# Kernel tuning notes

Hardware: AMD Instinct MI355X
Metric: run time of the kernel (lower is better)

Reference implementation:

```python
import jax, jax.numpy as jnp
import numpy as np

N_NODES = 100000
N_EDGES = 1600000
D_IN = 128
D_HID = 128
D_OUT = 64
N_GRAPHS = 128


def setup_inputs() -> dict:
    key = jax.random.key(0)
    ks = jax.random.split(key, 8)
    x = jax.random.normal(ks[0], (N_NODES, D_IN), dtype=jnp.float32)
    edge_index = jax.random.randint(ks[1], (2, N_EDGES), 0, N_NODES, dtype=jnp.int64)
    batch = jnp.sort(jax.random.randint(ks[2], (N_NODES,), 0, N_GRAPHS, dtype=jnp.int64))
    def glorot(k, fi, fo):
        s = jnp.sqrt(6.0 / (fi + fo)).astype(jnp.float32)
        return jax.random.uniform(k, (fi, fo), jnp.float32, -1.0, 1.0) * s
    return {
        "x": x, "edge_index": edge_index, "batch": batch,
        "W1": glorot(ks[3], D_IN, D_HID), "b1": jnp.zeros((D_HID,), jnp.float32),
        "W2": glorot(ks[4], D_HID, D_HID), "b2": jnp.zeros((D_HID,), jnp.float32),
        "W3": glorot(ks[5], D_HID, D_HID), "b3": jnp.zeros((D_HID,), jnp.float32),
        "Wfc": glorot(ks[6], D_HID, D_OUT), "bfc": jnp.zeros((D_OUT,), jnp.float32),
    }


def _gcn_graph(edge_index, n_nodes):
    # add self-loops and compute symmetric normalization (PyG gcn_norm)
    loop = jnp.arange(n_nodes, dtype=edge_index.dtype)
    src = jnp.concatenate([edge_index[0], loop])
    dst = jnp.concatenate([edge_index[1], loop])
    deg = jax.ops.segment_sum(jnp.ones_like(dst, dtype=jnp.float32), dst,
                              num_segments=n_nodes)
    dinv = jnp.where(deg > 0, jax.lax.rsqrt(deg), 0.0)
    norm = dinv[src] * dinv[dst]  # [E + N]
    return src, dst, norm


def _gcn_conv(x, src, dst, norm, W, b, n_nodes):
    h = x @ W                                    # [N, F_out]
    msg = h[src] * norm[:, None]                 # gather + scale
    agg = jax.ops.segment_sum(msg, dst, num_segments=n_nodes)  # scatter-add
    return agg + b


def reference(x, edge_index, batch, W1, b1, W2, b2, W3, b3, Wfc, bfc):
    n = x.shape[0]
    src, dst, norm = _gcn_graph(edge_index, n)
    h = jax.nn.relu(_gcn_conv(x, src, dst, norm, W1, b1, n))
    h = jax.nn.relu(_gcn_conv(h, src, dst, norm, W2, b2, n))
    h = jax.nn.relu(_gcn_conv(h, src, dst, norm, W3, b3, n))
    # global mean pool over graphs in the batch
    sums = jax.ops.segment_sum(h, batch, num_segments=N_GRAPHS)
    cnts = jax.ops.segment_sum(jnp.ones((n,), jnp.float32), batch,
                               num_segments=N_GRAPHS)
    pooled = sums / jnp.maximum(cnts, 1.0)[:, None]   # [G, D_HID]
    return pooled @ Wfc + bfc                         # [G, D_OUT]
```

## Files before the change

### kernel.cpp

```cpp
#include <hip/hip_runtime.h>

#define NN 100000
#define NE 1600000
#define DF 128
#define DOUT 64
#define NG 128
#define NB 391
#define EPB 2048
#define NBLKA ((NE + EPB - 1) / EPB)
#define NBLKX 6250
#define PCH 8
#define NAGB (NN / 16)

typedef short short8 __attribute__((ext_vector_type(8)));
typedef float floatx4 __attribute__((ext_vector_type(4)));
typedef float floatx2 __attribute__((ext_vector_type(2)));

__device__ __forceinline__ unsigned short f2bf(float f) {
    unsigned int b = __float_as_uint(f);
    unsigned int r = (b + 0x7fffu + ((b >> 16) & 1u)) >> 16;
    return (unsigned short)r;
}
__device__ __forceinline__ float bf2f_lo(unsigned int v) { return __uint_as_float(v << 16); }
__device__ __forceinline__ float bf2f_hi(unsigned int v) { return __uint_as_float(v & 0xffff0000u); }

__device__ __forceinline__ int phi(int p) {
    return (((p >> 6) << 2) + (p & 3)) * 16 + ((p >> 2) & 15);
}


__global__ __launch_bounds__(256) void k_init(int* __restrict__ bhist,
                                              const int* __restrict__ batch,
                                              int* __restrict__ gstart,
                                              const float* __restrict__ W1,
                                              const float* __restrict__ W2,
                                              const float* __restrict__ W3,
                                              unsigned short* __restrict__ O1,
                                              unsigned short* __restrict__ O2,
                                              unsigned short* __restrict__ O3) {
    int blk = blockIdx.x;
    if (blk < 2) {
        int i = blk * 256 + threadIdx.x;
        if (i < NB) bhist[i] = 0;
    } else if (blk == 2) {
        int g = threadIdx.x;
        if (g > NG) return;
        int lo = 0, hi = NN;
        while (lo < hi) {
            int mid = (lo + hi) >> 1;
            if (batch[mid] < g) lo = mid + 1; else hi = mid;
        }
        gstart[g] = lo;
    } else {
        int bb = blk - 3;
        const float* W = (bb >= 16) ? W3 : (bb >= 8) ? W2 : W1;
        unsigned short* O = (bb >= 16) ? O3 : (bb >= 8) ? O2 : O1;
        int idx = (bb & 7) * 256 + threadIdx.x;
        int l = idx & 63;
        int s = (idx >> 6) & 3;
        int tt = idx >> 8;
        int k0 = s * 32 + (l >> 4) * 8;
        int c = tt * 16 + (l & 15);
        unsigned short o[8];
#pragma unroll
        for (int j = 0; j < 8; j++) o[j] = f2bf(W[phi(k0 + j) * DF + c]);
        *(short8*)&O[idx * 8] = *(short8*)o;
    }
}


__global__ __launch_bounds__(256) void k_pre(const int* __restrict__ dst,
                                             int* __restrict__ bhist,
                                             const float* __restrict__ x,
                                             unsigned short* __restrict__ xb) {
    __shared__ int lh[NB];
    int t = threadIdx.x;
    if (blockIdx.x < NBLKA) {
        for (int i = t; i < NB; i += 256) lh[i] = 0;
        __syncthreads();
        int e0 = blockIdx.x * EPB;
        int e1 = min(e0 + EPB, NE);
        for (int e = e0 + t; e < e1; e += 256) atomicAdd(&lh[dst[e] >> 8], 1);
        __syncthreads();
        for (int i = t; i < NB; i += 256) {
            int c = lh[i];
            if (c) atomicAdd(&bhist[i], c);
        }
    } else {
        size_t i = ((size_t)(blockIdx.x - NBLKA) * 256 + t) * 8;
        size_t rb = i & ~(size_t)127;
        int p0 = (int)(i & 127);
        unsigned short o[8];
#pragma unroll
        for (int j = 0; j < 8; j++) o[j] = f2bf(x[rb + phi(p0 + j)]);
        *(short8*)&xb[i] = *(short8*)o;
    }
}

__global__ __launch_bounds__(512) void k_bscan(const int* __restrict__ bhist,
                                               int* __restrict__ bbase,
                                               int* __restrict__ bcur) {
    __shared__ int sh[512];
    int t = threadIdx.x;
    int v = (t < NB) ? bhist[t] : 0;
    sh[t] = v;
    __syncthreads();
    for (int off = 1; off < 512; off <<= 1) {
        int a = (t >= off) ? sh[t - off] : 0;
        __syncthreads();
        sh[t] += a;
        __syncthreads();
    }
    if (t < NB) {
        bbase[t] = sh[t] - v;
        bcur[t] = sh[t] - v;
    }
    if (t == NB - 1) bbase[NB] = sh[t];
}

__global__ __launch_bounds__(256) void k_pairs(const int* __restrict__ src,
                                               const int* __restrict__ dst,
                                               int* __restrict__ bcur,
                                               int2* __restrict__ ebuf) {
    __shared__ int lh[NB];
    __shared__ int lbase[NB];
    int t = threadIdx.x;
    for (int i = t; i < NB; i += 256) lh[i] = 0;
    __syncthreads();
    int e0 = blockIdx.x * EPB;
    int e1 = min(e0 + EPB, NE);
    for (int e = e0 + t; e < e1; e += 256) atomicAdd(&lh[dst[e] >> 8], 1);
    __syncthreads();
    for (int i = t; i < NB; i += 256) {
        int c = lh[i];
        lbase[i] = c ? atomicAdd(&bcur[i], c) : 0;
    }
    __syncthreads();
    for (int i = t; i < NB; i += 256) lh[i] = 0;
    __syncthreads();
    for (int e = e0 + t; e < e1; e += 256) {
        int s = src[e], d = dst[e];
        int bk = d >> 8;
        int off = atomicAdd(&lh[bk], 1);
        ebuf[lbase[bk] + off] = make_int2(s, d);
    }
}

__global__ __launch_bounds__(256) void k_build(const int2* __restrict__ ebuf,
                                               const int* __restrict__ bbase,
                                               int* __restrict__ rowptr,
                                               float* __restrict__ dinv,
                                               int* __restrict__ col) {
    __shared__ int deg[256];
    __shared__ int lst[256];
    int b = blockIdx.x, t = threadIdx.x;
    int n0 = b << 8;
    int node = n0 + t;
    deg[t] = 0;
    __syncthreads();
    int e0 = bbase[b], e1 = bbase[b + 1];
    for (int e = e0 + t; e < e1; e += 256) atomicAdd(&deg[ebuf[e].y - n0], 1);
    __syncthreads();
    int v = deg[t];
    lst[t] = v;
    __syncthreads();
    for (int off = 1; off < 256; off <<= 1) {
        int a = (t >= off) ? lst[t - off] : 0;
        __syncthreads();
        lst[t] += a;
        __syncthreads();
    }
    int mystart = e0 + lst[t] - v;
    if (node < NN) {
        rowptr[node] = mystart;
        dinv[node] = rsqrtf((float)(v + 1));
    }
    if (b == NB - 1 && t == 255) rowptr[NN] = e1;
    lst[t] = mystart;
    __syncthreads();
    for (int e = e0 + t; e < e1; e += 256) {
        int2 pr = ebuf[e];
        int p = atomicAdd(&lst[pr.y - n0], 1);
        col[p] = pr.x * DF;
    }
}


__global__ __launch_bounds__(256) void k_gemm(const unsigned short* __restrict__ X,
                                              const unsigned short* __restrict__ Wb,
                                              const float* __restrict__ dinv,
                                              unsigned char* __restrict__ fs8) {
    int t = threadIdx.x;
    int wave = t >> 6, l = t & 63;
    int r0 = blockIdx.x * 64 + wave * 16;
    int lm = l & 15, q = l >> 4;

    int arow = r0 + lm;
    if (arow >= NN) arow = NN - 1;
    const unsigned short* xrow = X + (size_t)arow * DF + q * 8;
    short8 af0 = *(const short8*)(xrow);
    short8 af1 = *(const short8*)(xrow + 32);
    short8 af2 = *(const short8*)(xrow + 64);
    short8 af3 = *(const short8*)(xrow + 96);

    int orow = r0 + q * 4;
    float dv[4];
#pragma unroll
    for (int j = 0; j < 4; j++) dv[j] = (orow + j < NN) ? dinv[orow + j] : 0.f;

    float res[4][8];
#pragma unroll
    for (int tt = 0; tt < 8; tt++) {
        floatx4 acc = {0.f, 0.f, 0.f, 0.f};
        const unsigned short* wp = Wb + ((size_t)(tt * 4) * 64 + l) * 8;
        acc = __builtin_amdgcn_mfma_f32_16x16x32_bf16(af0, *(const short8*)(wp), acc, 0, 0, 0);
        acc = __builtin_amdgcn_mfma_f32_16x16x32_bf16(af1, *(const short8*)(wp + 512), acc, 0, 0, 0);
        acc = __builtin_amdgcn_mfma_f32_16x16x32_bf16(af2, *(const short8*)(wp + 1024), acc, 0, 0, 0);
        acc = __builtin_amdgcn_mfma_f32_16x16x32_bf16(af3, *(const short8*)(wp + 1536), acc, 0, 0, 0);
#pragma unroll
        for (int j = 0; j < 4; j++) res[j][tt] = acc[j] * dv[j];
    }

#pragma unroll
    for (int g = 0; g < 2; g++) {
#pragma unroll
        for (int j = 0; j < 4; j++) {
            int r = orow + j;
            if (r >= NN) continue;
            unsigned int w8 = __builtin_amdgcn_cvt_pk_fp8_f32(res[j][g * 4 + 0], res[j][g * 4 + 1], 0, false);
            w8 = __builtin_amdgcn_cvt_pk_fp8_f32(res[j][g * 4 + 2], res[j][g * 4 + 3], w8, true);
            *(unsigned int*)&fs8[(size_t)r * DF + g * 64 + lm * 4] = w8;
        }
    }
}

__global__ __launch_bounds__(256) void k_agg(const unsigned char* __restrict__ fs8,
                                             const int* __restrict__ colb,
                                             const int* __restrict__ rowptr,
                                             const float* __restrict__ dinv,
                                             const float* __restrict__ b,
                                             unsigned short* __restrict__ out) {
    int w = (int)((blockIdx.x * (size_t)blockDim.x + threadIdx.x) >> 6);
    int lane = threadIdx.x & 63;
    int sub = lane >> 4;
    int fo = lane & 15;
    int foff = fo * 8;
    int n = w * 4 + sub;

    float bias[8];
#pragma unroll
    for (int j = 0; j < 8; j++) bias[j] = b[phi(foff + j)];
    float dvn = dinv[n];

    int e0 = rowptr[n], e1 = rowptr[n + 1];

    floatx2 acc0 = {0.f, 0.f}, acc1 = {0.f, 0.f}, acc2 = {0.f, 0.f}, acc3 = {0.f, 0.f};

    for (int base = e0; base < e1; base += 8) {
        int cb[8];
#pragma unroll
        for (int k = 0; k < 8; k++) cb[k] = colb[min(base + k, e1 - 1)];
        uint2 vv[8];
#pragma unroll
        for (int k = 0; k < 8; k++) vv[k] = *(const uint2*)&fs8[(size_t)cb[k] + foff];
#pragma unroll
        for (int k = 0; k < 8; k++) {
            if (base + k < e1) {
                acc0 += __builtin_amdgcn_cvt_pk_f32_fp8(vv[k].x, false);
                acc1 += __builtin_amdgcn_cvt_pk_f32_fp8(vv[k].x, true);
                acc2 += __builtin_amdgcn_cvt_pk_f32_fp8(vv[k].y, false);
                acc3 += __builtin_amdgcn_cvt_pk_f32_fp8(vv[k].y, true);
            }
        }
    }

    uint2 sv = *(const uint2*)&fs8[(size_t)n * DF + foff];
    acc0 += __builtin_amdgcn_cvt_pk_f32_fp8(sv.x, false);
    acc1 += __builtin_amdgcn_cvt_pk_f32_fp8(sv.x, true);
    acc2 += __builtin_amdgcn_cvt_pk_f32_fp8(sv.y, false);
    acc3 += __builtin_amdgcn_cvt_pk_f32_fp8(sv.y, true);

    float a[8] = {acc0.x, acc0.y, acc1.x, acc1.y, acc2.x, acc2.y, acc3.x, acc3.y};
    float o[8];
#pragma unroll
    for (int j = 0; j < 8; j++) o[j] = fmaxf(dvn * a[j] + bias[j], 0.f);
    uint4 pk;
    pk.x = (unsigned int)f2bf(o[0]) | ((unsigned int)f2bf(o[1]) << 16);
    pk.y = (unsigned int)f2bf(o[2]) | ((unsigned int)f2bf(o[3]) << 16);
    pk.z = (unsigned int)f2bf(o[4]) | ((unsigned int)f2bf(o[5]) << 16);
    pk.w = (unsigned int)f2bf(o[6]) | ((unsigned int)f2bf(o[7]) << 16);
    *(uint4*)&out[(size_t)n * DF + foff] = pk;
}


__global__ __launch_bounds__(256) void k_poolA(const unsigned short* __restrict__ h,
                                               const int* __restrict__ gstart,
                                               float* __restrict__ part) {
    __shared__ float2 red[256];
    int g = blockIdx.x >> 3, c = blockIdx.x & 7;
    int s = gstart[g], e = gstart[g + 1];
    int len = e - s;
    int cs = s + (int)(((long long)len * c) >> 3);
    int ce = s + (int)(((long long)len * (c + 1)) >> 3);
    int t = threadIdx.x;
    int fp = t & 63;
    int rs = t >> 6;
    float2 acc = make_float2(0.f, 0.f);
    for (int n = cs + rs; n < ce; n += 4) {
        unsigned int v = *(const unsigned int*)&h[(size_t)n * DF + fp * 2];
        acc.x += bf2f_lo(v);
        acc.y += bf2f_hi(v);
    }
    red[t] = acc;
    __syncthreads();
    if (rs == 0) {
        float2 a0 = red[fp], a1 = red[fp + 64], a2 = red[fp + 128], a3 = red[fp + 192];
        float2 o;
        o.x = (a0.x + a1.x) + (a2.x + a3.x);
        o.y = (a0.y + a1.y) + (a2.y + a3.y);
        *(float2*)&part[(size_t)blockIdx.x * DF + fp * 2] = o;
    }
}

__global__ __launch_bounds__(128) void k_poolfc(const float* __restrict__ part,
                                                const int* __restrict__ gstart,
                                                const float* __restrict__ Wfc,
                                                const float* __restrict__ bfc,
                                                float* __restrict__ out) {
    __shared__ float pl[DF];
    int g = blockIdx.x;
    int f = threadIdx.x;
    float s = 0.f;
#pragma unroll
    for (int c = 0; c < PCH; c++) s += part[(size_t)(g * PCH + c) * DF + f];
    int cnt = gstart[g + 1] - gstart[g];
    pl[phi(f)] = s / (float)max(cnt, 1);
    __syncthreads();
    if (f < DOUT) {
        float acc = bfc[f];
        for (int k = 0; k < DF; k++) acc += pl[k] * Wfc[k * DOUT + f];
        out[g * DOUT + f] = acc;
    }
}


extern "C" void kernel_launch(void* const* d_in, const int* in_sizes, int n_in,
                              void* d_out, int out_size, void* d_ws, size_t ws_size,
                              hipStream_t stream) {
    const float* x     = (const float*)d_in[0];
    const int*   ei    = (const int*)d_in[1];
    const int*   batch = (const int*)d_in[2];
    const float* W1 = (const float*)d_in[3];
    const float* b1 = (const float*)d_in[4];
    const float* W2 = (const float*)d_in[5];
    const float* b2 = (const float*)d_in[6];
    const float* W3 = (const float*)d_in[7];
    const float* b3 = (const float*)d_in[8];
    const float* Wfc = (const float*)d_in[9];
    const float* bfc = (const float*)d_in[10];
    float* out = (float*)d_out;

    char* p = (char*)d_ws;
    unsigned short* xb = (unsigned short*)p;  p += (size_t)NN * DF * sizeof(short);
    unsigned short* ob = (unsigned short*)p;  p += (size_t)NN * DF * sizeof(short);
    unsigned char*  fs8 = (unsigned char*)p;  p += (size_t)NN * DF;
    unsigned short* Wb1 = (unsigned short*)p; p += 16384 * sizeof(short);
    unsigned short* Wb2 = (unsigned short*)p; p += 16384 * sizeof(short);
    unsigned short* Wb3 = (unsigned short*)p; p += 16384 * sizeof(short);
    float* dinv = (float*)p;           p += (size_t)NN * sizeof(float);
    int* rowptr = (int*)p;             p += (size_t)(NN + 4) * sizeof(int);
    int* col    = (int*)p;             p += (size_t)NE * sizeof(int);
    int2* ebuf  = (int2*)p;            p += (size_t)NE * sizeof(int2);
    int* bhist  = (int*)p;             p += (size_t)(NB + 4) * sizeof(int);
    int* bbase  = (int*)p;             p += (size_t)(NB + 4) * sizeof(int);
    int* bcur   = (int*)p;             p += (size_t)(NB + 4) * sizeof(int);
    int* gstart = (int*)p;             p += (size_t)(NG + 4) * sizeof(int);
    float* part = (float*)p;           p += (size_t)NG * PCH * DF * sizeof(float);

    const int* e_src = ei;
    const int* e_dst = ei + NE;

    k_init<<<27, 256, 0, stream>>>(bhist, batch, gstart, W1, W2, W3, Wb1, Wb2, Wb3);
    k_pre<<<NBLKA + NBLKX, 256, 0, stream>>>(e_dst, bhist, x, xb);
    k_bscan<<<1, 512, 0, stream>>>(bhist, bbase, bcur);
    k_pairs<<<NBLKA, 256, 0, stream>>>(e_src, e_dst, bcur, ebuf);
    k_build<<<NB, 256, 0, stream>>>(ebuf, bbase, rowptr, dinv, col);

    int ggrid = (NN + 63) / 64;

    k_gemm<<<ggrid, 256, 0, stream>>>(xb, Wb1, dinv, fs8);
    k_agg<<<NAGB, 256, 0, stream>>>(fs8, col, rowptr, dinv, b1, ob);
    k_gemm<<<ggrid, 256, 0, stream>>>(ob, Wb2, dinv, fs8);
    k_agg<<<NAGB, 256, 0, stream>>>(fs8, col, rowptr, dinv, b2, ob);
    k_gemm<<<ggrid, 256, 0, stream>>>(ob, Wb3, dinv, fs8);
    k_agg<<<NAGB, 256, 0, stream>>>(fs8, col, rowptr, dinv, b3, ob);

    k_poolA<<<NG * PCH, 256, 0, stream>>>(ob, gstart, part);
    k_poolfc<<<NG, 128, 0, stream>>>(part, gstart, Wfc, bfc, out);
}
```

Before: 372.0 us.

## Replace global atomic bucket reservation with per-block histogram scan for edge bucketing

Each histogram block now writes its per-bucket counts to a global matrix instead of atomically adding into a global bucket histogram. A new per-bucket scan kernel computes deterministic per-block offsets, which lets the pair-writing kernel skip its second counting pass and its global atomics on the bucket cursors. Edges per block also grow from 2048 to 8192, which cuts the number of blocks to 196 so the scan fits in a 256-thread block. This adds a kernel launch and a hist matrix, and it reduces parallelism in the edge passes.

Measured after the change: 337.0 us. 9.4% less time.

```diff
diff --git a/kernel.cpp b/kernel.cpp
--- a/kernel.cpp
+++ b/kernel.cpp
@@ -6,7 +6,7 @@
 #define DOUT 64
 #define NG 128
 #define NB 391
-#define EPB 2048
+#define EPB 8192
 #define NBLKA ((NE + EPB - 1) / EPB)
 #define NBLKX 6250
 #define PCH 8
@@ -29,8 +29,7 @@
 }
 
 
-__global__ __launch_bounds__(256) void k_init(int* __restrict__ bhist,
-                                              const int* __restrict__ batch,
+__global__ __launch_bounds__(256) void k_init(const int* __restrict__ batch,
                                               int* __restrict__ gstart,
                                               const float* __restrict__ W1,
                                               const float* __restrict__ W2,
@@ -39,10 +38,7 @@
                                               unsigned short* __restrict__ O2,
                                               unsigned short* __restrict__ O3) {
     int blk = blockIdx.x;
-    if (blk < 2) {
-        int i = blk * 256 + threadIdx.x;
-        if (i < NB) bhist[i] = 0;
-    } else if (blk == 2) {
+    if (blk == 0) {
         int g = threadIdx.x;
         if (g > NG) return;
         int lo = 0, hi = NN;
@@ -52,7 +48,7 @@
         }
         gstart[g] = lo;
     } else {
-        int bb = blk - 3;
+        int bb = blk - 1;
         const float* W = (bb >= 16) ? W3 : (bb >= 8) ? W2 : W1;
         unsigned short* O = (bb >= 16) ? O3 : (bb >= 8) ? O2 : O1;
         int idx = (bb & 7) * 256 + threadIdx.x;
@@ -70,7 +66,7 @@
 
 
 __global__ __launch_bounds__(256) void k_pre(const int* __restrict__ dst,
-                                             int* __restrict__ bhist,
+                                             int* __restrict__ hist,
                                              const float* __restrict__ x,
                                              unsigned short* __restrict__ xb) {
     __shared__ int lh[NB];
@@ -82,10 +78,7 @@
         int e1 = min(e0 + EPB, NE);
         for (int e = e0 + t; e < e1; e += 256) atomicAdd(&lh[dst[e] >> 8], 1);
         __syncthreads();
-        for (int i = t; i < NB; i += 256) {
-            int c = lh[i];
-            if (c) atomicAdd(&bhist[i], c);
-        }
+        for (int i = t; i < NB; i += 256) hist[blockIdx.x * NB + i] = lh[i];
     } else {
         size_t i = ((size_t)(blockIdx.x - NBLKA) * 256 + t) * 8;
         size_t rb = i & ~(size_t)127;
@@ -97,9 +90,25 @@
     }
 }
 
+__global__ __launch_bounds__(256) void k_hscan(int* __restrict__ hist,
+                                               int* __restrict__ bhist) {
+    __shared__ int sh[256];
+    int b = blockIdx.x, t = threadIdx.x;
+    int v = (t < NBLKA) ? hist[t * NB + b] : 0;
+    sh[t] = v;
+    __syncthreads();
+    for (int off = 1; off < 256; off <<= 1) {
+        int a = (t >= off) ? sh[t - off] : 0;
+        __syncthreads();
+        sh[t] += a;
+        __syncthreads();
+    }
+    if (t < NBLKA) hist[t * NB + b] = sh[t] - v;
+    if (t == 255) bhist[b] = sh[255];
+}
+
 __global__ __launch_bounds__(512) void k_bscan(const int* __restrict__ bhist,
-                                               int* __restrict__ bbase,
-                                               int* __restrict__ bcur) {
+                                               int* __restrict__ bbase) {
     __shared__ int sh[512];
     int t = threadIdx.x;
     int v = (t < NB) ? bhist[t] : 0;
@@ -111,33 +120,25 @@
         sh[t] += a;
         __syncthreads();
     }
-    if (t < NB) {
-        bbase[t] = sh[t] - v;
-        bcur[t] = sh[t] - v;
-    }
+    if (t < NB) bbase[t] = sh[t] - v;
     if (t == NB - 1) bbase[NB] = sh[t];
 }
 
 __global__ __launch_bounds__(256) void k_pairs(const int* __restrict__ src,
                                                const int* __restrict__ dst,
-                                               int* __restrict__ bcur,
+                                               const int* __restrict__ hist,
+                                               const int* __restrict__ bbase,
                                                int2* __restrict__ ebuf) {
     __shared__ int lh[NB];
     __shared__ int lbase[NB];
     int t = threadIdx.x;
-    for (int i = t; i < NB; i += 256) lh[i] = 0;
+    for (int i = t; i < NB; i += 256) {
+        lh[i] = 0;
+        lbase[i] = bbase[i] + hist[blockIdx.x * NB + i];
+    }
     __syncthreads();
     int e0 = blockIdx.x * EPB;
     int e1 = min(e0 + EPB, NE);
-    for (int e = e0 + t; e < e1; e += 256) atomicAdd(&lh[dst[e] >> 8], 1);
-    __syncthreads();
-    for (int i = t; i < NB; i += 256) {
-        int c = lh[i];
-        lbase[i] = c ? atomicAdd(&bcur[i], c) : 0;
-    }
-    __syncthreads();
-    for (int i = t; i < NB; i += 256) lh[i] = 0;
-    __syncthreads();
     for (int e = e0 + t; e < e1; e += 256) {
         int s = src[e], d = dst[e];
         int bk = d >> 8;
@@ -373,17 +374,18 @@
     int2* ebuf  = (int2*)p;            p += (size_t)NE * sizeof(int2);
     int* bhist  = (int*)p;             p += (size_t)(NB + 4) * sizeof(int);
     int* bbase  = (int*)p;             p += (size_t)(NB + 4) * sizeof(int);
-    int* bcur   = (int*)p;             p += (size_t)(NB + 4) * sizeof(int);
+    int* hist   = (int*)p;             p += (size_t)NBLKA * NB * sizeof(int);
     int* gstart = (int*)p;             p += (size_t)(NG + 4) * sizeof(int);
     float* part = (float*)p;           p += (size_t)NG * PCH * DF * sizeof(float);
 
     const int* e_src = ei;
     const int* e_dst = ei + NE;
 
-    k_init<<<27, 256, 0, stream>>>(bhist, batch, gstart, W1, W2, W3, Wb1, Wb2, Wb3);
-    k_pre<<<NBLKA + NBLKX, 256, 0, stream>>>(e_dst, bhist, x, xb);
-    k_bscan<<<1, 512, 0, stream>>>(bhist, bbase, bcur);
-    k_pairs<<<NBLKA, 256, 0, stream>>>(e_src, e_dst, bcur, ebuf);
+    k_init<<<25, 256, 0, stream>>>(batch, gstart, W1, W2, W3, Wb1, Wb2, Wb3);
+    k_pre<<<NBLKA + NBLKX, 256, 0, stream>>>(e_dst, hist, x, xb);
+    k_hscan<<<NB, 256, 0, stream>>>(hist, bhist);
+    k_bscan<<<1, 512, 0, stream>>>(bhist, bbase);
+    k_pairs<<<NBLKA, 256, 0, stream>>>(e_src, e_dst, hist, bbase, ebuf);
     k_build<<<NB, 256, 0, stream>>>(ebuf, bbase, rowptr, dinv, col);
 
     int ggrid = (NN + 63) / 64;
```
